# Kernel optimization log

Measured on AMD Instinct MI355X. Metric: run time of the kernel, lower is better.

The kernel has to match this reference:

```python
import jax, jax.numpy as jnp
import numpy as np

DECAY = 0.99
EPS = 1e-5


def setup_inputs() -> dict:
    key = jax.random.key(0)
    k1, k2 = jax.random.split(key)
    inp = jax.random.normal(k1, (32, 64, 64, 64), dtype=jnp.float32)  # [B,H,W,dim]
    embed = jax.random.normal(k2, (64, 512), dtype=jnp.float32)       # [dim, n_embed]
    cluster_size = jnp.zeros((512,), dtype=jnp.float32)
    embed_avg = embed  # buffer initialized as embed.clone() in torch
    return {"input": inp, "embed": embed, "cluster_size": cluster_size, "embed_avg": embed_avg}


def reference(input, embed, cluster_size, embed_avg):
    dim, n_embed = embed.shape
    flatten = input.reshape(-1, dim)  # [N, dim]

    # pairwise squared distances via ||f||^2 - 2 f.E + ||E||^2 -> [N, n_embed]
    dist = ((flatten ** 2).sum(1, keepdims=True)
            - 2.0 * flatten @ embed
            + (embed ** 2).sum(0, keepdims=True))
    embed_ind_flat = jnp.argmin(dist, axis=1)  # [N] (== argmax of -dist)

    # codebook lookup (F.embedding on embed.T)
    quantize = jnp.take(embed.T, embed_ind_flat, axis=0).reshape(input.shape)

    # EMA stats: one-hot sum and one-hot @ flatten expressed as scatter-adds
    ones = jnp.ones_like(embed_ind_flat, dtype=flatten.dtype)
    embed_onehot_sum = jax.ops.segment_sum(ones, embed_ind_flat, num_segments=n_embed)      # [n_embed]
    embed_sum = jax.ops.segment_sum(flatten, embed_ind_flat, num_segments=n_embed).T       # [dim, n_embed]

    new_cluster_size = cluster_size * DECAY + (1.0 - DECAY) * embed_onehot_sum
    new_embed_avg = embed_avg * DECAY + (1.0 - DECAY) * embed_sum
    n = new_cluster_size.sum()
    cs = (new_cluster_size + EPS) / (n + n_embed * EPS) * n
    new_embed = new_embed_avg / cs[None, :]

    diff = ((jax.lax.stop_gradient(quantize) - input) ** 2).mean()
    quantize_st = input + jax.lax.stop_gradient(quantize - input)  # straight-through
    embed_ind = embed_ind_flat.reshape(input.shape[:-1])

    return (quantize_st, diff, embed_ind, new_cluster_size, new_embed_avg, new_embed)
```

## Files before the change

kernel.cpp:

```cpp
#include <hip/hip_runtime.h>

typedef __attribute__((ext_vector_type(8))) short short8_t;
typedef __attribute__((ext_vector_type(4))) float f32x4;

#define N_ROWS   131072
#define DIM      64
#define NE       512
#define DECAYF   0.99f
#define OMDECAY  0.01f
#define EPSF     1e-5f
#define GAP_THR  0.02f

#define Q_OFF    0
#define DIFF_OFF 8388608
#define IND_OFF  8388609
#define CS_OFF   8519681
#define AVG_OFF  8520193
#define EMB_OFF  8552961

#define WS_ET      0
#define WS_ENORM   32768
#define WS_EN64    33280
#define WS_CSDIV   34304
#define WS_DIFF    34816
#define WS_RCNT    34817
#define WS_IDX     34818
#define WS_RLIST   165890
#define WS_BH      296964
#define WS_BL      313348
#define WS_HIST    329732
#define WS_BINBASE 330244
#define WS_CURSOR  330756
#define WS_SORTED  331268
#define WS_ACCUM   462340

__device__ __forceinline__ ushort f32_to_bf16_rn(float f) {
    unsigned u = __float_as_uint(f);
    unsigned r = (u + 0x7FFFu + ((u >> 16) & 1u)) >> 16;
    return (ushort)r;
}
__device__ __forceinline__ float bf16_to_f32(ushort h) {
    return __uint_as_float(((unsigned)h) << 16);
}

__global__ __launch_bounds__(512) void prep1_kernel(const float* __restrict__ embed,
                                                    float* __restrict__ ws) {
    const int d = blockIdx.x;
    const int c = threadIdx.x;
    float v = embed[d * NE + c];
    ws[WS_ET + c * DIM + d] = v;

    ushort hb = f32_to_bf16_rn(v);
    float  lf = v - bf16_to_f32(hb);
    ushort lb = f32_to_bf16_rn(lf);

    const int T  = c >> 4;
    const int n  = c & 15;
    const int s  = d >> 5;
    const int k8 = (d >> 3) & 3;
    const int jj = d & 7;
    const int l  = k8 * 16 + n;
    const int idx = (T * 2 + s) * 512 + l * 8 + jj;
    ((ushort*)(ws + WS_BH))[idx] = hb;
    ((ushort*)(ws + WS_BL))[idx] = lb;

    if (d == 0 && c == 0) {
        ws[WS_DIFF] = 0.0f;
        ((int*)ws)[WS_RCNT] = 0;
    }
    if (d == 1) ((int*)ws)[WS_HIST + c] = 0;
    ws[WS_ACCUM + blockIdx.x * 512 + threadIdx.x] = 0.0f;
}

__global__ __launch_bounds__(256) void prep2_kernel(float* __restrict__ ws) {
    const int jcode = blockIdx.x * 4 + (threadIdx.x >> 6);
    const int d     = threadIdx.x & 63;
    float v = ws[WS_ET + jcode * DIM + d];
    double sq = (double)v * (double)v;
    #pragma unroll
    for (int off = 32; off > 0; off >>= 1) sq += __shfl_down(sq, off, 64);
    if (d == 0) {
        ws[WS_ENORM + jcode] = (float)sq;
        ((double*)(ws + WS_EN64))[jcode] = sq;
    }
}

__global__ __launch_bounds__(256) void dist_kernel(const float* __restrict__ input,
                                                   float* __restrict__ ws) {
    const int tid  = threadIdx.x;
    const int lane = tid & 63;
    const int wv   = tid >> 6;
    const int r0   = blockIdx.x * 128 + wv * 32;
    const int n15  = lane & 15;
    const int koff = (lane >> 4) * 8;

    short8_t Ahi[2][2], Alo[2][2];
    #pragma unroll
    for (int sub = 0; sub < 2; sub++) {
        const float* rp = input + (size_t)(r0 + sub * 16 + n15) * DIM + koff;
        #pragma unroll
        for (int s = 0; s < 2; s++) {
            float4 x0 = *(const float4*)(rp + s * 32);
            float4 x1 = *(const float4*)(rp + s * 32 + 4);
            float xf[8] = {x0.x, x0.y, x0.z, x0.w, x1.x, x1.y, x1.z, x1.w};
            short8_t h, l;
            #pragma unroll
            for (int e = 0; e < 8; e++) {
                ushort hb = f32_to_bf16_rn(xf[e]);
                float  lf = xf[e] - bf16_to_f32(hb);
                ushort lb = f32_to_bf16_rn(lf);
                h[e] = (short)hb;
                l[e] = (short)lb;
            }
            Ahi[sub][s] = h;
            Alo[sub][s] = l;
        }
    }

    const ushort* bhp = (const ushort*)(ws + WS_BH) + lane * 8;
    const ushort* blp = (const ushort*)(ws + WS_BL) + lane * 8;

    float m1[8], m2[8];
    int   j1[8];
    #pragma unroll
    for (int i = 0; i < 8; i++) { m1[i] = 3.4e38f; m2[i] = 3.4e38f; j1[i] = 0; }

    #pragma unroll 2
    for (int T = 0; T < 32; T++) {
        short8_t Bh0 = *(const short8_t*)(bhp + T * 1024);
        short8_t Bh1 = *(const short8_t*)(bhp + T * 1024 + 512);
        short8_t Bl0 = *(const short8_t*)(blp + T * 1024);
        short8_t Bl1 = *(const short8_t*)(blp + T * 1024 + 512);

        f32x4 aa = {0.f, 0.f, 0.f, 0.f};
        f32x4 ab = {0.f, 0.f, 0.f, 0.f};
        aa = __builtin_amdgcn_mfma_f32_16x16x32_bf16(Ahi[0][0], Bh0, aa, 0, 0, 0);
        ab = __builtin_amdgcn_mfma_f32_16x16x32_bf16(Ahi[1][0], Bh0, ab, 0, 0, 0);
        aa = __builtin_amdgcn_mfma_f32_16x16x32_bf16(Alo[0][0], Bh0, aa, 0, 0, 0);
        ab = __builtin_amdgcn_mfma_f32_16x16x32_bf16(Alo[1][0], Bh0, ab, 0, 0, 0);
        aa = __builtin_amdgcn_mfma_f32_16x16x32_bf16(Ahi[0][0], Bl0, aa, 0, 0, 0);
        ab = __builtin_amdgcn_mfma_f32_16x16x32_bf16(Ahi[1][0], Bl0, ab, 0, 0, 0);
        aa = __builtin_amdgcn_mfma_f32_16x16x32_bf16(Ahi[0][1], Bh1, aa, 0, 0, 0);
        ab = __builtin_amdgcn_mfma_f32_16x16x32_bf16(Ahi[1][1], Bh1, ab, 0, 0, 0);
        aa = __builtin_amdgcn_mfma_f32_16x16x32_bf16(Alo[0][1], Bh1, aa, 0, 0, 0);
        ab = __builtin_amdgcn_mfma_f32_16x16x32_bf16(Alo[1][1], Bh1, ab, 0, 0, 0);
        aa = __builtin_amdgcn_mfma_f32_16x16x32_bf16(Ahi[0][1], Bl1, aa, 0, 0, 0);
        ab = __builtin_amdgcn_mfma_f32_16x16x32_bf16(Ahi[1][1], Bl1, ab, 0, 0, 0);

        const float en = ws[WS_ENORM + T * 16 + n15];
        const int   jc = T * 16 + n15;
        #pragma unroll
        for (int q = 0; q < 4; q++) {
            float da = fmaf(-2.0f, aa[q], en);
            m2[q]    = fminf(m2[q], fmaxf(m1[q], da));
            j1[q]    = (da < m1[q]) ? jc : j1[q];
            m1[q]    = fminf(m1[q], da);
            float db = fmaf(-2.0f, ab[q], en);
            m2[q+4]  = fminf(m2[q+4], fmaxf(m1[q+4], db));
            j1[q+4]  = (db < m1[q+4]) ? jc : j1[q+4];
            m1[q+4]  = fminf(m1[q+4], db);
        }
    }

    #pragma unroll
    for (int off = 1; off < 16; off <<= 1) {
        #pragma unroll
        for (int i = 0; i < 8; i++) {
            float b1 = __shfl_xor(m1[i], off, 64);
            float b2 = __shfl_xor(m2[i], off, 64);
            int   bj = __shfl_xor(j1[i], off, 64);
            float a1 = m1[i];
            float nm2 = fminf(fminf(m2[i], b2), fmaxf(a1, b1));
            bool takeB = (b1 < a1) || (b1 == a1 && bj < j1[i]);
            m1[i] = takeB ? b1 : a1;
            j1[i] = takeB ? bj : j1[i];
            m2[i] = nm2;
        }
    }

    if (n15 == 0) {
        #pragma unroll
        for (int i = 0; i < 8; i++) {
            int sub = i >> 2, q = i & 3;
            int r = r0 + sub * 16 + (lane >> 4) * 4 + q;
            ((int*)ws)[WS_IDX + r] = j1[i];
            if (m2[i] - m1[i] < GAP_THR) {
                int pos = atomicAdd((int*)ws + WS_RCNT, 1);
                ((int*)ws)[WS_RLIST + pos] = r;
            }
        }
    }
}

__global__ __launch_bounds__(256) void refine_kernel(const float* __restrict__ input,
                                                     float* __restrict__ ws) {
    __shared__ float rowf[4][DIM];
    const int cnt  = ((const int*)ws)[WS_RCNT];
    const int lane = threadIdx.x & 63;
    const int wv   = threadIdx.x >> 6;
    const double* en64 = (const double*)(ws + WS_EN64);

    for (int ii = blockIdx.x * 4 + wv; ii < cnt; ii += 2048) {
        const int r = ((const int*)ws)[WS_RLIST + ii];
        rowf[wv][lane] = input[(size_t)r * DIM + lane];
        double bd = 1e300;
        int    bj = 0x7fffffff;
        for (int kk = 0; kk < 8; kk++) {
            int j = kk * 64 + lane;
            const float* ep = ws + WS_ET + j * DIM;
            double s0 = 0.0, s1 = 0.0;
            #pragma unroll 8
            for (int d = 0; d < DIM; d += 2) {
                s0 = fma((double)ep[d],     (double)rowf[wv][d],     s0);
                s1 = fma((double)ep[d + 1], (double)rowf[wv][d + 1], s1);
            }
            double dist = en64[j] - 2.0 * (s0 + s1);
            if (dist < bd || (dist == bd && j < bj)) { bd = dist; bj = j; }
        }
        #pragma unroll
        for (int off = 32; off > 0; off >>= 1) {
            double od = __shfl_down(bd, off, 64);
            int    oj = __shfl_down(bj, off, 64);
            if (od < bd || (od == bd && oj < bj)) { bd = od; bj = oj; }
        }
        if (lane == 0) ((int*)ws)[WS_IDX + r] = bj;
    }
}

__global__ __launch_bounds__(256) void hist_kernel(float* __restrict__ ws) {
    __shared__ int hist[NE];
    const int tid = threadIdx.x;
    for (int e = tid; e < NE; e += 256) hist[e] = 0;
    __syncthreads();

    const int4 j4 = *((const int4*)((const int*)ws + WS_IDX) + blockIdx.x * 256 + tid);
    atomicAdd(&hist[j4.x], 1);
    atomicAdd(&hist[j4.y], 1);
    atomicAdd(&hist[j4.z], 1);
    atomicAdd(&hist[j4.w], 1);
    __syncthreads();

    for (int e = tid; e < NE; e += 256) {
        int h = hist[e];
        if (h) atomicAdd((int*)ws + WS_HIST + e, h);
    }
}

__global__ __launch_bounds__(512) void scanfin_kernel(const float* __restrict__ cluster_size,
                                                      float* __restrict__ ws,
                                                      float* __restrict__ out) {
    __shared__ int wsums[8];
    __shared__ float red[8];
    const int t    = threadIdx.x;
    const int lane = t & 63;
    const int wv   = t >> 6;
    const int v    = ((const int*)ws)[WS_HIST + t];
    const float csnew = fmaf(cluster_size[t], DECAYF, OMDECAY * (float)v);
    out[CS_OFF + t] = csnew;

    int x = v;
    #pragma unroll
    for (int off = 1; off < 64; off <<= 1) {
        int y = __shfl_up(x, off, 64);
        if (lane >= off) x += y;
    }
    if (lane == 63) wsums[wv] = x;

    float s = csnew;
    #pragma unroll
    for (int off = 32; off > 0; off >>= 1) s += __shfl_down(s, off, 64);
    if (lane == 0) red[wv] = s;
    __syncthreads();

    int add = 0;
    for (int w = 0; w < wv; w++) add += wsums[w];
    const int excl = x + add - v;
    ((int*)ws)[WS_BINBASE + t] = excl;
    ((int*)ws)[WS_CURSOR + t]  = excl;

    float n = red[0] + red[1] + red[2] + red[3] + red[4] + red[5] + red[6] + red[7];
    ws[WS_CSDIV + t] = (csnew + EPSF) / (n + (float)NE * EPSF) * n;
}

__global__ __launch_bounds__(256) void place_kernel(float* __restrict__ ws) {
    __shared__ int lhist[NE];
    __shared__ int lbase[NE];
    __shared__ int lcur[NE];
    const int tid  = threadIdx.x;
    const int base = blockIdx.x * 256;

    for (int e = tid; e < NE; e += 256) { lhist[e] = 0; lcur[e] = 0; }
    __syncthreads();

    const int r = base + tid;
    const int j = ((const int*)ws)[WS_IDX + r];
    atomicAdd(&lhist[j], 1);
    __syncthreads();

    for (int e = tid; e < NE; e += 256)
        if (lhist[e]) lbase[e] = atomicAdd((int*)ws + WS_CURSOR + e, lhist[e]);
    __syncthreads();

    const int pos = lbase[j] + atomicAdd(&lcur[j], 1);
    ((int*)ws)[WS_SORTED + pos] = r;
}

__global__ __launch_bounds__(256) void sum_kernel(const float* __restrict__ input,
                                                  float* __restrict__ ws,
                                                  float* __restrict__ out) {
    __shared__ float wred[4];
    const int lane = threadIdx.x & 63;
    const int wv   = threadIdx.x >> 6;
    const int i0   = (blockIdx.x * 4 + wv) * 32;

    const int rv = ((const int*)ws)[WS_SORTED + i0 + (lane & 31)];
    const int jv = ((const int*)ws)[WS_IDX + rv];

    float acc  = 0.0f;
    float dacc = 0.0f;
    int   jcur = __shfl(jv, 0, 64);

    #pragma unroll
    for (int k = 0; k < 32; k += 8) {
        int   rr[8], jj[8];
        float v[8], q[8];
        #pragma unroll
        for (int u = 0; u < 8; u++) {
            rr[u] = __shfl(rv, k + u, 64);
            jj[u] = __shfl(jv, k + u, 64);
        }
        #pragma unroll
        for (int u = 0; u < 8; u++) v[u] = input[(size_t)rr[u] * DIM + lane];
        #pragma unroll
        for (int u = 0; u < 8; u++) q[u] = ws[WS_ET + jj[u] * DIM + lane];

        #pragma unroll
        for (int u = 0; u < 8; u++) {
            out[Q_OFF + (size_t)rr[u] * DIM + lane] = q[u];
            float dd = q[u] - v[u];
            dacc = fmaf(dd, dd, dacc);
            if (lane == 0) out[IND_OFF + rr[u]] = (float)jj[u];
            if (jj[u] != jcur) {
                atomicAdd(&ws[WS_ACCUM + jcur * DIM + lane], acc);
                acc = 0.0f;
                jcur = jj[u];
            }
            acc += v[u];
        }
    }
    atomicAdd(&ws[WS_ACCUM + jcur * DIM + lane], acc);

    #pragma unroll
    for (int off = 1; off < 64; off <<= 1) dacc += __shfl_xor(dacc, off, 64);
    if (lane == 0) wred[wv] = dacc;
    __syncthreads();
    if (threadIdx.x == 0)
        atomicAdd(&ws[WS_DIFF], wred[0] + wred[1] + wred[2] + wred[3]);
}

__global__ __launch_bounds__(512) void emaout_kernel(const float* __restrict__ embed_avg,
                                                     const float* __restrict__ ws,
                                                     float* __restrict__ out) {
    const int e = blockIdx.x * 512 + threadIdx.x;
    const int d = e >> 9;
    const int j = e & (NE - 1);
    float s   = ws[WS_ACCUM + j * DIM + d];
    float avg = fmaf(embed_avg[e], DECAYF, OMDECAY * s);
    out[AVG_OFF + e] = avg;
    out[EMB_OFF + e] = avg / ws[WS_CSDIV + j];
    if (e == 0) out[DIFF_OFF] = ws[WS_DIFF] * (1.0f / 8388608.0f);
}

extern "C" void kernel_launch(void* const* d_in, const int* in_sizes, int n_in,
                              void* d_out, int out_size, void* d_ws, size_t ws_size,
                              hipStream_t stream) {
    const float* input        = (const float*)d_in[0];
    const float* embed        = (const float*)d_in[1];
    const float* cluster_size = (const float*)d_in[2];
    const float* embed_avg    = (const float*)d_in[3];
    float* out = (float*)d_out;
    float* ws  = (float*)d_ws;

    prep1_kernel<<<64, 512, 0, stream>>>(embed, ws);
    prep2_kernel<<<128, 256, 0, stream>>>(ws);
    dist_kernel<<<N_ROWS / 128, 256, 0, stream>>>(input, ws);
    refine_kernel<<<512, 256, 0, stream>>>(input, ws);
    hist_kernel<<<128, 256, 0, stream>>>(ws);
    scanfin_kernel<<<1, 512, 0, stream>>>(cluster_size, ws, out);
    place_kernel<<<512, 256, 0, stream>>>(ws);
    sum_kernel<<<N_ROWS / 128, 256, 0, stream>>>(input, ws, out);
    emaout_kernel<<<64, 512, 0, stream>>>(embed_avg, ws, out);
}
```

Before: 118.3 us.

## Merge prep kernels and fuse histogram, scan and placement into cooperative kernel

Folds the two codebook prep kernels into a single launch of 512 single-wave blocks. Replaces the histogram, single-block scan and placement kernels with one cooperative kernel that uses two grid-wide syncs, so each block's local histogram stays in shared memory for the placement step. This removes several kernel launches and a re-read of the index array. In exchange it relies on all 512 blocks being co-resident, and grid.sync carries its own barrier cost.

After: 219.2 us. 85.2% more time.

```diff
diff --git a/kernel.cpp b/kernel.cpp
--- a/kernel.cpp
+++ b/kernel.cpp
@@ -1,4 +1,7 @@
 #include <hip/hip_runtime.h>
+#include <hip/hip_cooperative_groups.h>
+
+namespace cg = cooperative_groups;
 
 typedef __attribute__((ext_vector_type(8))) short short8_t;
 typedef __attribute__((ext_vector_type(4))) float f32x4;
@@ -43,10 +46,10 @@
     return __uint_as_float(((unsigned)h) << 16);
 }
 
-__global__ __launch_bounds__(512) void prep1_kernel(const float* __restrict__ embed,
-                                                    float* __restrict__ ws) {
-    const int d = blockIdx.x;
-    const int c = threadIdx.x;
+__global__ __launch_bounds__(64) void prep_kernel(const float* __restrict__ embed,
+                                                  float* __restrict__ ws) {
+    const int c = blockIdx.x;
+    const int d = threadIdx.x;
     float v = embed[d * NE + c];
     ws[WS_ET + c * DIM + d] = v;
 
@@ -64,25 +67,19 @@
     ((ushort*)(ws + WS_BH))[idx] = hb;
     ((ushort*)(ws + WS_BL))[idx] = lb;
 
-    if (d == 0 && c == 0) {
-        ws[WS_DIFF] = 0.0f;
-        ((int*)ws)[WS_RCNT] = 0;
-    }
-    if (d == 1) ((int*)ws)[WS_HIST + c] = 0;
-    ws[WS_ACCUM + blockIdx.x * 512 + threadIdx.x] = 0.0f;
-}
-
-__global__ __launch_bounds__(256) void prep2_kernel(float* __restrict__ ws) {
-    const int jcode = blockIdx.x * 4 + (threadIdx.x >> 6);
-    const int d     = threadIdx.x & 63;
-    float v = ws[WS_ET + jcode * DIM + d];
     double sq = (double)v * (double)v;
     #pragma unroll
     for (int off = 32; off > 0; off >>= 1) sq += __shfl_down(sq, off, 64);
     if (d == 0) {
-        ws[WS_ENORM + jcode] = (float)sq;
-        ((double*)(ws + WS_EN64))[jcode] = sq;
-    }
+        ws[WS_ENORM + c] = (float)sq;
+        ((double*)(ws + WS_EN64))[c] = sq;
+        ((int*)ws)[WS_HIST + c] = 0;
+        if (c == 0) {
+            ws[WS_DIFF] = 0.0f;
+            ((int*)ws)[WS_RCNT] = 0;
+        }
+    }
+    ws[WS_ACCUM + c * DIM + d] = 0.0f;
 }
 
 __global__ __launch_bounds__(256) void dist_kernel(const float* __restrict__ input,
@@ -227,65 +224,16 @@
     }
 }
 
-__global__ __launch_bounds__(256) void hist_kernel(float* __restrict__ ws) {
-    __shared__ int hist[NE];
-    const int tid = threadIdx.x;
-    for (int e = tid; e < NE; e += 256) hist[e] = 0;
-    __syncthreads();
-
-    const int4 j4 = *((const int4*)((const int*)ws + WS_IDX) + blockIdx.x * 256 + tid);
-    atomicAdd(&hist[j4.x], 1);
-    atomicAdd(&hist[j4.y], 1);
-    atomicAdd(&hist[j4.z], 1);
-    atomicAdd(&hist[j4.w], 1);
-    __syncthreads();
-
-    for (int e = tid; e < NE; e += 256) {
-        int h = hist[e];
-        if (h) atomicAdd((int*)ws + WS_HIST + e, h);
-    }
-}
-
-__global__ __launch_bounds__(512) void scanfin_kernel(const float* __restrict__ cluster_size,
-                                                      float* __restrict__ ws,
-                                                      float* __restrict__ out) {
-    __shared__ int wsums[8];
-    __shared__ float red[8];
-    const int t    = threadIdx.x;
-    const int lane = t & 63;
-    const int wv   = t >> 6;
-    const int v    = ((const int*)ws)[WS_HIST + t];
-    const float csnew = fmaf(cluster_size[t], DECAYF, OMDECAY * (float)v);
-    out[CS_OFF + t] = csnew;
-
-    int x = v;
-    #pragma unroll
-    for (int off = 1; off < 64; off <<= 1) {
-        int y = __shfl_up(x, off, 64);
-        if (lane >= off) x += y;
-    }
-    if (lane == 63) wsums[wv] = x;
-
-    float s = csnew;
-    #pragma unroll
-    for (int off = 32; off > 0; off >>= 1) s += __shfl_down(s, off, 64);
-    if (lane == 0) red[wv] = s;
-    __syncthreads();
-
-    int add = 0;
-    for (int w = 0; w < wv; w++) add += wsums[w];
-    const int excl = x + add - v;
-    ((int*)ws)[WS_BINBASE + t] = excl;
-    ((int*)ws)[WS_CURSOR + t]  = excl;
-
-    float n = red[0] + red[1] + red[2] + red[3] + red[4] + red[5] + red[6] + red[7];
-    ws[WS_CSDIV + t] = (csnew + EPSF) / (n + (float)NE * EPSF) * n;
-}
-
-__global__ __launch_bounds__(256) void place_kernel(float* __restrict__ ws) {
+__global__ __launch_bounds__(256) void coop_hsp_kernel(float* __restrict__ ws,
+                                                       const float* __restrict__ cluster_size,
+                                                       float* __restrict__ out) {
+    cg::grid_group grid = cg::this_grid();
     __shared__ int lhist[NE];
     __shared__ int lbase[NE];
     __shared__ int lcur[NE];
+    __shared__ int wsums[4];
+    __shared__ float red[4];
+
     const int tid  = threadIdx.x;
     const int base = blockIdx.x * 256;
 
@@ -296,6 +244,55 @@
     const int j = ((const int*)ws)[WS_IDX + r];
     atomicAdd(&lhist[j], 1);
     __syncthreads();
+
+    for (int e = tid; e < NE; e += 256) {
+        int h = lhist[e];
+        if (h) atomicAdd((int*)ws + WS_HIST + e, h);
+    }
+
+    grid.sync();
+
+    if (blockIdx.x == 0) {
+        const int lane = tid & 63;
+        const int wv   = tid >> 6;
+        const int b0 = 2 * tid, b1 = 2 * tid + 1;
+        const int h0 = ((const int*)ws)[WS_HIST + b0];
+        const int h1 = ((const int*)ws)[WS_HIST + b1];
+        const float cs0 = fmaf(cluster_size[b0], DECAYF, OMDECAY * (float)h0);
+        const float cs1 = fmaf(cluster_size[b1], DECAYF, OMDECAY * (float)h1);
+        out[CS_OFF + b0] = cs0;
+        out[CS_OFF + b1] = cs1;
+
+        int p = h0 + h1;
+        int x = p;
+        #pragma unroll
+        for (int off = 1; off < 64; off <<= 1) {
+            int y = __shfl_up(x, off, 64);
+            if (lane >= off) x += y;
+        }
+        if (lane == 63) wsums[wv] = x;
+
+        float s = cs0 + cs1;
+        #pragma unroll
+        for (int off = 32; off > 0; off >>= 1) s += __shfl_down(s, off, 64);
+        if (lane == 0) red[wv] = s;
+        __syncthreads();
+
+        int add = 0;
+        for (int w = 0; w < wv; w++) add += wsums[w];
+        const int excl0 = x + add - p;
+        const int excl1 = excl0 + h0;
+        ((int*)ws)[WS_BINBASE + b0] = excl0;
+        ((int*)ws)[WS_CURSOR + b0]  = excl0;
+        ((int*)ws)[WS_BINBASE + b1] = excl1;
+        ((int*)ws)[WS_CURSOR + b1]  = excl1;
+
+        float n = red[0] + red[1] + red[2] + red[3];
+        ws[WS_CSDIV + b0] = (cs0 + EPSF) / (n + (float)NE * EPSF) * n;
+        ws[WS_CSDIV + b1] = (cs1 + EPSF) / (n + (float)NE * EPSF) * n;
+    }
+
+    grid.sync();
 
     for (int e = tid; e < NE; e += 256)
         if (lhist[e]) lbase[e] = atomicAdd((int*)ws + WS_CURSOR + e, lhist[e]);
@@ -381,13 +378,14 @@
     float* out = (float*)d_out;
     float* ws  = (float*)d_ws;
 
-    prep1_kernel<<<64, 512, 0, stream>>>(embed, ws);
-    prep2_kernel<<<128, 256, 0, stream>>>(ws);
+    prep_kernel<<<512, 64, 0, stream>>>(embed, ws);
     dist_kernel<<<N_ROWS / 128, 256, 0, stream>>>(input, ws);
     refine_kernel<<<512, 256, 0, stream>>>(input, ws);
-    hist_kernel<<<128, 256, 0, stream>>>(ws);
-    scanfin_kernel<<<1, 512, 0, stream>>>(cluster_size, ws, out);
-    place_kernel<<<512, 256, 0, stream>>>(ws);
+
+    void* cargs[] = { (void*)&ws, (void*)&cluster_size, (void*)&out };
+    hipLaunchCooperativeKernel((void*)coop_hsp_kernel, dim3(512), dim3(256),
+                               cargs, 0, stream);
+
     sum_kernel<<<N_ROWS / 128, 256, 0, stream>>>(input, ws, out);
     emaout_kernel<<<64, 512, 0, stream>>>(embed_avg, ws, out);
 }
```
